# Optimization experiments

Hardware: AMD Instinct MI355X
Metric: run time of the kernel (lower is better)

Reference implementation:

```python
import jax, jax.numpy as jnp
import numpy as np

ALPHA_MIN = float(np.exp(-1.0 / 5.0))
ALPHA_MAX = float(np.exp(-1.0 / 25.0))
B, T, F_IN, H = 32, 1000, 700, 512

# Boxcar surrogate spike: forward heaviside, backward pass-through on |x|<=0.5
@jax.custom_vjp
def spike(x):
    return (x > 0).astype(x.dtype)

def _spike_fwd(x):
    return (x > 0).astype(x.dtype), x

def _spike_bwd(x, g):
    return (jnp.where(jnp.abs(x) <= 0.5, g, jnp.zeros_like(g)),)

spike.defvjp(_spike_fwd, _spike_bwd)

def _ortho(k, n):
    a = jax.random.normal(k, (n, n))
    q, r = jnp.linalg.qr(a)
    return (q * jnp.sign(jnp.diag(r))[None, :]).astype(jnp.float32)

def setup_inputs() -> dict:
    key = jax.random.key(0)
    ks = jax.random.split(key, 14)
    return {
        "x": jax.random.normal(ks[0], (B, T, F_IN), dtype=jnp.float32),
        "W0": jax.random.normal(ks[1], (H, F_IN), dtype=jnp.float32) / np.sqrt(F_IN),
        "V0": _ortho(ks[2], H),
        "alpha0": jax.random.uniform(ks[3], (H,), minval=ALPHA_MIN, maxval=ALPHA_MAX, dtype=jnp.float32),
        "W1": jax.random.normal(ks[4], (H, H), dtype=jnp.float32) / np.sqrt(H),
        "V1": _ortho(ks[5], H),
        "alpha1": jax.random.uniform(ks[6], (H,), minval=ALPHA_MIN, maxval=ALPHA_MAX, dtype=jnp.float32),
        "Wr": jax.random.normal(ks[7], (H, H), dtype=jnp.float32) / np.sqrt(H),
        "alphar": jax.random.uniform(ks[8], (H,), minval=ALPHA_MIN, maxval=ALPHA_MAX, dtype=jnp.float32),
        "ut0_0": jax.random.uniform(ks[9], (B, H), dtype=jnp.float32),
        "st0_0": jax.random.uniform(ks[10], (B, H), dtype=jnp.float32),
        "ut0_1": jax.random.uniform(ks[11], (B, H), dtype=jnp.float32),
        "st0_1": jax.random.uniform(ks[12], (B, H), dtype=jnp.float32),
        "ut0_r": jax.random.uniform(ks[13], (B, H), dtype=jnp.float32),
    }

def _rlif(Wx, V, alpha, ut0, st0):
    # Wx: [B, T, H]; recurrent V with zeroed diagonal, st @ V as in torch source
    a = jnp.clip(alpha, ALPHA_MIN, ALPHA_MAX)
    Vz = V * (1.0 - jnp.eye(V.shape[0], dtype=V.dtype))
    def step(carry, wx_t):
        ut, st = carry
        ut = a * (ut - st) + (1.0 - a) * (wx_t + st @ Vz)
        st = spike(ut - 1.0)  # threshold = 1.0
        return (ut, st), st
    _, s = jax.lax.scan(step, (ut0, st0), jnp.swapaxes(Wx, 0, 1))  # [T, B, H]
    return jnp.swapaxes(s, 0, 1)  # [B, T, H]

def _readout(Wx, alpha, ut0):
    a = jnp.clip(alpha, ALPHA_MIN, ALPHA_MAX)
    def step(ut, wx_t):
        ut = a * ut + (1.0 - a) * wx_t
        return ut, jax.nn.softmax(ut, axis=-1)
    _, ps = jax.lax.scan(step, ut0, jnp.swapaxes(Wx, 0, 1))
    return ps.sum(axis=0)  # [B, H]

def reference(x, W0, V0, alpha0, W1, V1, alpha1, Wr, alphar, ut0_0, st0_0, ut0_1, st0_1, ut0_r):
    s0 = _rlif(jnp.einsum('btf,hf->bth', x, W0), V0, alpha0, ut0_0, st0_0)
    s1 = _rlif(jnp.einsum('bth,gh->btg', s0, W1), V1, alpha1, ut0_1, st0_1)
    out = _readout(jnp.einsum('bth,gh->btg', s1, Wr), alphar, ut0_r)
    firing_rates = jnp.concatenate([s0, s1], axis=2).mean(axis=(0, 1))  # [2H]
    return out, firing_rates
```

## Files before the change

### kernel.cpp

```cpp
#include <hip/hip_runtime.h>

#define H_   512
#define T_   1000
#define B_   32
#define FIN_ 700
#define C_   50
#define L_   20
#define PF_  4

typedef _Float16 h2v __attribute__((ext_vector_type(2)));
typedef _Float16 h4v __attribute__((ext_vector_type(4)));

static __device__ __forceinline__ float clampAlpha(float a) {
    const float AMIN = 0.8187307530779818f;
    const float AMAX = 0.9607894391523232f;
    return fminf(fmaxf(a, AMIN), AMAX);
}

__global__ __launch_bounds__(256) void vconv_kernel(
    const float* __restrict__ V, _Float16* __restrict__ Vh)
{
    const int i = (blockIdx.x * 256 + threadIdx.x) * 4;
    const float4 v = *reinterpret_cast<const float4*>(V + i);
    h4v o;
    o.x = (_Float16)v.x; o.y = (_Float16)v.y;
    o.z = (_Float16)v.z; o.w = (_Float16)v.w;
    *reinterpret_cast<h4v*>(Vh + i) = o;
}

__global__ __launch_bounds__(256) void gemm_bt_kernel(
    const float* __restrict__ A, const float* __restrict__ Bt,
    float* __restrict__ C, int M, int N, int K)
{
    __shared__ __align__(16) float As[16][68];
    __shared__ __align__(16) float Bs[16][68];
    const int tid = threadIdx.x;
    const int bm = blockIdx.x * 64;
    const int bn = blockIdx.y * 64;
    const int tx = tid & 15, ty = tid >> 4;
    const int lrow = tid >> 2;
    const int lk   = (tid & 3) << 2;
    float acc[4][4] = {};
    const float* Arow = A + (size_t)(bm + lrow) * K;
    const float* Brow = Bt + (size_t)(bn + lrow) * K;

    for (int k0 = 0; k0 < K; k0 += 16) {
        const int ka = k0 + lk;
        float4 av, bv;
        if (ka + 3 < K) {
            av = *reinterpret_cast<const float4*>(Arow + ka);
            bv = *reinterpret_cast<const float4*>(Brow + ka);
        } else {
            float a_[4], b_[4];
            #pragma unroll
            for (int i = 0; i < 4; ++i) {
                a_[i] = (ka + i < K) ? Arow[ka + i] : 0.f;
                b_[i] = (ka + i < K) ? Brow[ka + i] : 0.f;
            }
            av = make_float4(a_[0], a_[1], a_[2], a_[3]);
            bv = make_float4(b_[0], b_[1], b_[2], b_[3]);
        }
        __syncthreads();
        As[lk + 0][lrow] = av.x; As[lk + 1][lrow] = av.y;
        As[lk + 2][lrow] = av.z; As[lk + 3][lrow] = av.w;
        Bs[lk + 0][lrow] = bv.x; Bs[lk + 1][lrow] = bv.y;
        Bs[lk + 2][lrow] = bv.z; Bs[lk + 3][lrow] = bv.w;
        __syncthreads();
        #pragma unroll
        for (int kk = 0; kk < 16; ++kk) {
            const float4 a4 = *reinterpret_cast<const float4*>(&As[kk][ty << 2]);
            const float4 b4 = *reinterpret_cast<const float4*>(&Bs[kk][tx << 2]);
            const float aa[4] = {a4.x, a4.y, a4.z, a4.w};
            const float bb[4] = {b4.x, b4.y, b4.z, b4.w};
            #pragma unroll
            for (int i = 0; i < 4; ++i)
                #pragma unroll
                for (int j = 0; j < 4; ++j)
                    acc[i][j] = fmaf(aa[i], bb[j], acc[i][j]);
        }
    }
    #pragma unroll
    for (int i = 0; i < 4; ++i) {
        const float4 r = make_float4(acc[i][0], acc[i][1], acc[i][2], acc[i][3]);
        *reinterpret_cast<float4*>(&C[(size_t)(bm + ty * 4 + i) * N + bn + tx * 4]) = r;
    }
}

__global__ __launch_bounds__(256) void rlif_kernel(
    const float* __restrict__ Wx,
    const _Float16* __restrict__ Vh,
    const float* __restrict__ alpha,
    const float* __restrict__ ut0,
    const float* __restrict__ st0,
    float* __restrict__ s_out,
    float* __restrict__ fire)
{
    const int b    = blockIdx.x;
    const int tid  = threadIdx.x;
    const int j0   = tid * 2;
    const int wid  = tid >> 6;
    const int lane = tid & 63;
    __shared__ __align__(16) int act[2][4][132];
    __shared__ int cnt[2][4];
    __shared__ float st0_sh[H_];

    const float a0 = clampAlpha(alpha[j0]);
    const float a1 = clampAlpha(alpha[j0 + 1]);
    const float om0 = 1.f - a0, om1 = 1.f - a1;
    const float vd0 = (float)Vh[(size_t)j0 * H_ + j0];
    const float vd1 = (float)Vh[(size_t)(j0 + 1) * H_ + (j0 + 1)];
    float u0 = ut0[b * H_ + j0], u1 = ut0[b * H_ + j0 + 1];
    float s0 = st0[b * H_ + j0], s1 = st0[b * H_ + j0 + 1];
    float f0 = 0.f, f1 = 0.f;
    const float* wxb = Wx + (size_t)b * T_ * H_;
    float*       sob = s_out + (size_t)b * T_ * H_;

    if (tid < 8) ((int*)cnt)[tid] = 0;
    st0_sh[j0]     = st0[b * H_ + j0];
    st0_sh[j0 + 1] = st0[b * H_ + j0 + 1];
    __syncthreads();

    float pre0 = 0.f, pre1 = 0.f;
    #pragma unroll 8
    for (int h = 0; h < H_; ++h) {
        const float s = st0_sh[h];
        const h2v v = *reinterpret_cast<const h2v*>(&Vh[(size_t)h * H_ + j0]);
        pre0 = fmaf(s, (float)v.x, pre0);
        pre1 = fmaf(s, (float)v.y, pre1);
    }

    float2 wxp[PF_];
    #pragma unroll
    for (int i = 0; i < PF_; ++i)
        wxp[i] = *reinterpret_cast<const float2*>(&wxb[(size_t)i * H_ + j0]);

    int p = 0;
    for (int g = 0; g < T_ / PF_; ++g) {
        #pragma unroll
        for (int i = 0; i < PF_; ++i) {
            const int t = g * PF_ + i;
            const float2 wx = wxp[i];
            if (t + PF_ < T_)
                wxp[i] = *reinterpret_cast<const float2*>(&wxb[(size_t)(t + PF_) * H_ + j0]);

            float rec0 = 0.f, rec1 = 0.f;
            #pragma unroll
            for (int seg = 0; seg < 4; ++seg) {
                const int n = __builtin_amdgcn_readfirstlane(cnt[p][seg]);
                const int* ap = &act[p][seg][0];
                int k = 0;
                for (; k + 4 <= n; k += 4) {
                    const int4 h4 = *reinterpret_cast<const int4*>(ap + k);
                    const h2v v0 = *reinterpret_cast<const h2v*>(&Vh[(size_t)h4.x * H_ + j0]);
                    const h2v v1 = *reinterpret_cast<const h2v*>(&Vh[(size_t)h4.y * H_ + j0]);
                    const h2v v2 = *reinterpret_cast<const h2v*>(&Vh[(size_t)h4.z * H_ + j0]);
                    const h2v v3 = *reinterpret_cast<const h2v*>(&Vh[(size_t)h4.w * H_ + j0]);
                    rec0 += ((float)v0.x + (float)v1.x) + ((float)v2.x + (float)v3.x);
                    rec1 += ((float)v0.y + (float)v1.y) + ((float)v2.y + (float)v3.y);
                }
                for (; k < n; ++k) {
                    const h2v v = *reinterpret_cast<const h2v*>(&Vh[(size_t)ap[k] * H_ + j0]);
                    rec0 += (float)v.x; rec1 += (float)v.y;
                }
            }
            if (t == 0) { rec0 = pre0; rec1 = pre1; }
            rec0 -= s0 * vd0;
            rec1 -= s1 * vd1;

            u0 = a0 * (u0 - s0) + om0 * (wx.x + rec0);
            u1 = a1 * (u1 - s1) + om1 * (wx.y + rec1);
            s0 = (u0 > 1.f) ? 1.f : 0.f;
            s1 = (u1 > 1.f) ? 1.f : 0.f;
            f0 += s0; f1 += s1;
            *reinterpret_cast<float2*>(&sob[(size_t)t * H_ + j0]) = make_float2(s0, s1);

            const unsigned long long bal0 = __ballot(u0 > 1.f);
            const unsigned long long bal1 = __ballot(u1 > 1.f);
            const unsigned long long lt = (lane == 63) ? 0x7FFFFFFFFFFFFFFFULL
                                                       : ((1ULL << lane) - 1ULL);
            int k = (int)__popcll(bal0 & lt) + (int)__popcll(bal1 & lt);
            int* seg = &act[p ^ 1][wid][0];
            if (s0 != 0.f) { seg[k] = j0; ++k; }
            if (s1 != 0.f) { seg[k] = j0 + 1; }
            if (lane == 0) cnt[p ^ 1][wid] = (int)__popcll(bal0) + (int)__popcll(bal1);

            asm volatile("s_waitcnt lgkmcnt(0)" ::: "memory");
            __builtin_amdgcn_s_barrier();
            __builtin_amdgcn_sched_barrier(0);
            p ^= 1;
        }
    }
    fire[b * H_ + j0]     = f0;
    fire[b * H_ + j0 + 1] = f1;
}

__global__ __launch_bounds__(256) void ro_partial_kernel(
    const float* __restrict__ Wx,
    const float* __restrict__ alpha,
    float* __restrict__ u_end)
{
    const int b = blockIdx.x;
    const int c = blockIdx.y;
    const int j0 = threadIdx.x * 2;
    const float a0 = clampAlpha(alpha[j0]);
    const float a1 = clampAlpha(alpha[j0 + 1]);
    const float om0 = 1.f - a0, om1 = 1.f - a1;
    float u0 = 0.f, u1 = 0.f;
    const float* wxb = Wx + ((size_t)b * T_ + (size_t)c * L_) * H_;
    #pragma unroll 4
    for (int t = 0; t < L_; ++t) {
        const float2 wx = *reinterpret_cast<const float2*>(&wxb[(size_t)t * H_ + j0]);
        u0 = fmaf(a0, u0, om0 * wx.x);
        u1 = fmaf(a1, u1, om1 * wx.y);
    }
    float* ue = u_end + ((size_t)b * C_ + c) * H_;
    *reinterpret_cast<float2*>(&ue[j0]) = make_float2(u0, u1);
}

__global__ __launch_bounds__(256) void ro_carry_kernel(
    const float* __restrict__ u_end,
    const float* __restrict__ alpha,
    const float* __restrict__ ut0,
    float* __restrict__ carry)
{
    const int b = blockIdx.x;
    const int j0 = threadIdx.x * 2;
    const float a0 = clampAlpha(alpha[j0]);
    const float a1 = clampAlpha(alpha[j0 + 1]);
    const float aL0 = powf(a0, (float)L_);
    const float aL1 = powf(a1, (float)L_);
    float c0 = ut0[b * H_ + j0];
    float c1 = ut0[b * H_ + j0 + 1];
    for (int c = 0; c < C_; ++c) {
        float* cr = carry + ((size_t)b * C_ + c) * H_;
        *reinterpret_cast<float2*>(&cr[j0]) = make_float2(c0, c1);
        const float2 ue = *reinterpret_cast<const float2*>(
            &u_end[((size_t)b * C_ + c) * H_ + j0]);
        c0 = fmaf(aL0, c0, ue.x);
        c1 = fmaf(aL1, c1, ue.y);
    }
}

__global__ __launch_bounds__(256) void ro_softmax_kernel(
    const float* __restrict__ Wx,
    const float* __restrict__ alpha,
    const float* __restrict__ carry,
    float* __restrict__ opart)
{
    const int b = blockIdx.x;
    const int c = blockIdx.y;
    const int tid = threadIdx.x;
    const int j0 = tid * 2;
    __shared__ float red[8];
    const float a0 = clampAlpha(alpha[j0]);
    const float a1 = clampAlpha(alpha[j0 + 1]);
    const float om0 = 1.f - a0, om1 = 1.f - a1;
    float2 u = *reinterpret_cast<const float2*>(
        &carry[((size_t)b * C_ + c) * H_ + j0]);
    float u0 = u.x, u1 = u.y;
    float o0 = 0.f, o1 = 0.f;
    const float* wxb = Wx + ((size_t)b * T_ + (size_t)c * L_) * H_;
    const int wave = tid >> 6;
    const int lane = tid & 63;

    for (int t = 0; t < L_; ++t) {
        const float2 wx = *reinterpret_cast<const float2*>(&wxb[(size_t)t * H_ + j0]);
        u0 = fmaf(a0, u0, om0 * wx.x);
        u1 = fmaf(a1, u1, om1 * wx.y);
        float m = fmaxf(u0, u1);
        #pragma unroll
        for (int off = 32; off > 0; off >>= 1)
            m = fmaxf(m, __shfl_xor(m, off, 64));
        if (lane == 0) red[wave] = m;
        __syncthreads();
        m = fmaxf(fmaxf(red[0], red[1]), fmaxf(red[2], red[3]));
        const float e0 = expf(u0 - m), e1 = expf(u1 - m);
        float sum = e0 + e1;
        #pragma unroll
        for (int off = 32; off > 0; off >>= 1)
            sum += __shfl_xor(sum, off, 64);
        if (lane == 0) red[4 + wave] = sum;
        __syncthreads();
        sum = (red[4] + red[5]) + (red[6] + red[7]);
        const float inv = 1.f / sum;
        o0 = fmaf(e0, inv, o0);
        o1 = fmaf(e1, inv, o1);
        __syncthreads();
    }
    float* op = opart + ((size_t)c * B_ + b) * H_;
    *reinterpret_cast<float2*>(&op[j0]) = make_float2(o0, o1);
}

__global__ __launch_bounds__(256) void ro_reduce_kernel(
    const float* __restrict__ opart, float* __restrict__ out)
{
    const int idx = blockIdx.x * 256 + threadIdx.x;
    float s = 0.f;
    for (int c = 0; c < C_; ++c) s += opart[(size_t)c * B_ * H_ + idx];
    out[idx] = s;
}

__global__ __launch_bounds__(256) void fire_reduce_kernel(
    const float* __restrict__ fire, float* __restrict__ out)
{
    const int h = blockIdx.x * 256 + threadIdx.x;
    if (h >= H_) return;
    const float inv = 1.f / (float)(B_ * T_);
    float s = 0.f;
    for (int b = 0; b < B_; ++b) s += fire[b * H_ + h];
    out[h] = s * inv;
    s = 0.f;
    for (int b = 0; b < B_; ++b) s += fire[B_ * H_ + b * H_ + h];
    out[H_ + h] = s * inv;
}

extern "C" void kernel_launch(void* const* d_in, const int* in_sizes, int n_in,
                              void* d_out, int out_size, void* d_ws, size_t ws_size,
                              hipStream_t stream)
{
    const float* x      = (const float*)d_in[0];
    const float* W0     = (const float*)d_in[1];
    const float* V0     = (const float*)d_in[2];
    const float* alpha0 = (const float*)d_in[3];
    const float* W1     = (const float*)d_in[4];
    const float* V1     = (const float*)d_in[5];
    const float* alpha1 = (const float*)d_in[6];
    const float* Wr     = (const float*)d_in[7];
    const float* alphar = (const float*)d_in[8];
    const float* ut0_0  = (const float*)d_in[9];
    const float* st0_0  = (const float*)d_in[10];
    const float* ut0_1  = (const float*)d_in[11];
    const float* st0_1  = (const float*)d_in[12];
    const float* ut0_r  = (const float*)d_in[13];
    float* out = (float*)d_out;

    const size_t NBTH = (size_t)B_ * T_ * H_;
    const size_t NBCH = (size_t)B_ * C_ * H_;
    float* buf0  = (float*)d_ws;
    float* buf1  = buf0 + NBTH;
    float* fire  = buf1 + NBTH;
    float* u_end = fire + 2 * B_ * H_;
    float* carry = u_end + NBCH;
    float* opart = carry + NBCH;
    _Float16* V0h = (_Float16*)(opart + (size_t)C_ * B_ * H_);
    _Float16* V1h = V0h + (size_t)H_ * H_;

    vconv_kernel<<<(H_ * H_) / 1024, 256, 0, stream>>>(V0, V0h);
    vconv_kernel<<<(H_ * H_) / 1024, 256, 0, stream>>>(V1, V1h);

    dim3 gG(32000 / 64, 512 / 64);
    gemm_bt_kernel<<<gG, 256, 0, stream>>>(x, W0, buf0, 32000, 512, 700);
    rlif_kernel<<<32, 256, 0, stream>>>(buf0, V0h, alpha0, ut0_0, st0_0, buf1, fire);
    gemm_bt_kernel<<<gG, 256, 0, stream>>>(buf1, W1, buf0, 32000, 512, 512);
    rlif_kernel<<<32, 256, 0, stream>>>(buf0, V1h, alpha1, ut0_1, st0_1, buf1, fire + B_ * H_);
    gemm_bt_kernel<<<gG, 256, 0, stream>>>(buf1, Wr, buf0, 32000, 512, 512);
    ro_partial_kernel<<<dim3(B_, C_), 256, 0, stream>>>(buf0, alphar, u_end);
    ro_carry_kernel<<<B_, 256, 0, stream>>>(u_end, alphar, ut0_r, carry);
    ro_softmax_kernel<<<dim3(B_, C_), 256, 0, stream>>>(buf0, alphar, carry, opart);
    ro_reduce_kernel<<<(B_ * H_) / 256, 256, 0, stream>>>(opart, out);
    fire_reduce_kernel<<<2, 256, 0, stream>>>(fire, out + B_ * H_);
}
```

Baseline: 1.748 ms.

## Fuse both RLIF layers and sparse spike-driven projections into one pipelined kernel

Replaces the two per-layer RLIF kernels and the two dense GEMMs on spike tensors (W1, Wr) with one kernel. It computes layer-1 input and readout input as sparse gathers over transposed fp16 weight rows indexed by active spikes, and skews layer 1 by one step so both recurrences share a single barrier per step. This removes two 32000x512x512 GEMMs, the separate launch of the second sequential scan, and the spike-tensor writes and reads. Each step now does more gather work per thread, and W1/Wr are rounded to fp16. Workspace is reused, with the readout buffers aliasing buf0.

```diff
diff --git a/kernel.cpp b/kernel.cpp
--- a/kernel.cpp
+++ b/kernel.cpp
@@ -3,7 +3,6 @@
 #define H_   512
 #define T_   1000
 #define B_   32
-#define FIN_ 700
 #define C_   50
 #define L_   20
 #define PF_  4
@@ -26,6 +25,21 @@
     o.x = (_Float16)v.x; o.y = (_Float16)v.y;
     o.z = (_Float16)v.z; o.w = (_Float16)v.w;
     *reinterpret_cast<h4v*>(Vh + i) = o;
+}
+
+__global__ __launch_bounds__(256) void tconv_kernel(
+    const float* __restrict__ W, _Float16* __restrict__ Wt)
+{
+    __shared__ float tile[32][33];
+    const int bx = blockIdx.x * 32, by = blockIdx.y * 32;
+    const int tx = threadIdx.x & 31, ty = threadIdx.x >> 5;
+    #pragma unroll
+    for (int r = 0; r < 32; r += 8)
+        tile[ty + r][tx] = W[(size_t)(by + ty + r) * H_ + bx + tx];
+    __syncthreads();
+    #pragma unroll
+    for (int r = 0; r < 32; r += 8)
+        Wt[(size_t)(bx + ty + r) * H_ + by + tx] = (_Float16)tile[tx][ty + r];
 }
 
 __global__ __launch_bounds__(256) void gemm_bt_kernel(
@@ -86,13 +100,16 @@
     }
 }
 
-__global__ __launch_bounds__(256) void rlif_kernel(
-    const float* __restrict__ Wx,
-    const _Float16* __restrict__ Vh,
-    const float* __restrict__ alpha,
-    const float* __restrict__ ut0,
-    const float* __restrict__ st0,
-    float* __restrict__ s_out,
+__global__ __launch_bounds__(256) void fused_snn_kernel(
+    const float* __restrict__ Wx0,
+    const _Float16* __restrict__ V0h,
+    const _Float16* __restrict__ W1th,
+    const _Float16* __restrict__ V1h,
+    const _Float16* __restrict__ Wrth,
+    const float* __restrict__ alpha0, const float* __restrict__ alpha1,
+    const float* __restrict__ ut00, const float* __restrict__ st00,
+    const float* __restrict__ ut01, const float* __restrict__ st01,
+    float* __restrict__ wxr,
     float* __restrict__ fire)
 {
     const int b    = blockIdx.x;
@@ -100,34 +117,57 @@
     const int j0   = tid * 2;
     const int wid  = tid >> 6;
     const int lane = tid & 63;
-    __shared__ __align__(16) int act[2][4][132];
-    __shared__ int cnt[2][4];
-    __shared__ float st0_sh[H_];
-
-    const float a0 = clampAlpha(alpha[j0]);
-    const float a1 = clampAlpha(alpha[j0 + 1]);
-    const float om0 = 1.f - a0, om1 = 1.f - a1;
-    const float vd0 = (float)Vh[(size_t)j0 * H_ + j0];
-    const float vd1 = (float)Vh[(size_t)(j0 + 1) * H_ + (j0 + 1)];
-    float u0 = ut0[b * H_ + j0], u1 = ut0[b * H_ + j0 + 1];
-    float s0 = st0[b * H_ + j0], s1 = st0[b * H_ + j0 + 1];
-    float f0 = 0.f, f1 = 0.f;
-    const float* wxb = Wx + (size_t)b * T_ * H_;
-    float*       sob = s_out + (size_t)b * T_ * H_;
-
-    if (tid < 8) ((int*)cnt)[tid] = 0;
-    st0_sh[j0]     = st0[b * H_ + j0];
-    st0_sh[j0 + 1] = st0[b * H_ + j0 + 1];
+    __shared__ __align__(16) int act0[2][4][132];
+    __shared__ __align__(16) int act1[2][4][132];
+    __shared__ int cnt0[2][4];
+    __shared__ int cnt1[2][4];
+    __shared__ float sh[H_];
+
+    const float a0a = clampAlpha(alpha0[j0]);
+    const float a0b = clampAlpha(alpha0[j0 + 1]);
+    const float om0a = 1.f - a0a, om0b = 1.f - a0b;
+    const float a1a = clampAlpha(alpha1[j0]);
+    const float a1b = clampAlpha(alpha1[j0 + 1]);
+    const float om1a = 1.f - a1a, om1b = 1.f - a1b;
+    const float vd0a = (float)V0h[(size_t)j0 * H_ + j0];
+    const float vd0b = (float)V0h[(size_t)(j0 + 1) * H_ + j0 + 1];
+    const float vd1a = (float)V1h[(size_t)j0 * H_ + j0];
+    const float vd1b = (float)V1h[(size_t)(j0 + 1) * H_ + j0 + 1];
+
+    float u0a = ut00[b * H_ + j0], u0b = ut00[b * H_ + j0 + 1];
+    float s0a = st00[b * H_ + j0], s0b = st00[b * H_ + j0 + 1];
+    float u1a = ut01[b * H_ + j0], u1b = ut01[b * H_ + j0 + 1];
+    float s1a = st01[b * H_ + j0], s1b = st01[b * H_ + j0 + 1];
+    float f0a = 0.f, f0b = 0.f, f1a = 0.f, f1b = 0.f;
+
+    const float* wxb  = Wx0 + (size_t)b * T_ * H_;
+    float*       wxrb = wxr + (size_t)b * T_ * H_;
+
+    if (tid < 8)               ((int*)cnt0)[tid] = 0;
+    if (tid >= 8 && tid < 16)  ((int*)cnt1)[tid - 8] = 0;
+
+    sh[j0] = s0a; sh[j0 + 1] = s0b;
     __syncthreads();
-
-    float pre0 = 0.f, pre1 = 0.f;
+    float pre0a = 0.f, pre0b = 0.f;
     #pragma unroll 8
     for (int h = 0; h < H_; ++h) {
-        const float s = st0_sh[h];
-        const h2v v = *reinterpret_cast<const h2v*>(&Vh[(size_t)h * H_ + j0]);
-        pre0 = fmaf(s, (float)v.x, pre0);
-        pre1 = fmaf(s, (float)v.y, pre1);
-    }
+        const float s = sh[h];
+        const h2v v = *reinterpret_cast<const h2v*>(&V0h[(size_t)h * H_ + j0]);
+        pre0a = fmaf(s, (float)v.x, pre0a);
+        pre0b = fmaf(s, (float)v.y, pre0b);
+    }
+    __syncthreads();
+    sh[j0] = s1a; sh[j0 + 1] = s1b;
+    __syncthreads();
+    float pre1a = 0.f, pre1b = 0.f;
+    #pragma unroll 8
+    for (int h = 0; h < H_; ++h) {
+        const float s = sh[h];
+        const h2v v = *reinterpret_cast<const h2v*>(&V1h[(size_t)h * H_ + j0]);
+        pre1a = fmaf(s, (float)v.x, pre1a);
+        pre1b = fmaf(s, (float)v.y, pre1b);
+    }
+    __syncthreads();
 
     float2 wxp[PF_];
     #pragma unroll
@@ -135,54 +175,113 @@
         wxp[i] = *reinterpret_cast<const float2*>(&wxb[(size_t)i * H_ + j0]);
 
     int p = 0;
-    for (int g = 0; g < T_ / PF_; ++g) {
+    for (int g = 0; g < (T_ + 2 + PF_ - 1) / PF_; ++g) {
         #pragma unroll
-        for (int i = 0; i < PF_; ++i) {
-            const int t = g * PF_ + i;
-            const float2 wx = wxp[i];
-            if (t + PF_ < T_)
-                wxp[i] = *reinterpret_cast<const float2*>(&wxb[(size_t)(t + PF_) * H_ + j0]);
-
-            float rec0 = 0.f, rec1 = 0.f;
+        for (int i4 = 0; i4 < PF_; ++i4) {
+            const int i = g * PF_ + i4;
+            if (i > T_ + 1) break;
+
+            float r0a = 0.f, r0b = 0.f, w1a = 0.f, w1b = 0.f;
             #pragma unroll
             for (int seg = 0; seg < 4; ++seg) {
-                const int n = __builtin_amdgcn_readfirstlane(cnt[p][seg]);
-                const int* ap = &act[p][seg][0];
+                const int n = __builtin_amdgcn_readfirstlane(cnt0[p][seg]);
+                const int* ap = &act0[p][seg][0];
                 int k = 0;
                 for (; k + 4 <= n; k += 4) {
                     const int4 h4 = *reinterpret_cast<const int4*>(ap + k);
-                    const h2v v0 = *reinterpret_cast<const h2v*>(&Vh[(size_t)h4.x * H_ + j0]);
-                    const h2v v1 = *reinterpret_cast<const h2v*>(&Vh[(size_t)h4.y * H_ + j0]);
-                    const h2v v2 = *reinterpret_cast<const h2v*>(&Vh[(size_t)h4.z * H_ + j0]);
-                    const h2v v3 = *reinterpret_cast<const h2v*>(&Vh[(size_t)h4.w * H_ + j0]);
-                    rec0 += ((float)v0.x + (float)v1.x) + ((float)v2.x + (float)v3.x);
-                    rec1 += ((float)v0.y + (float)v1.y) + ((float)v2.y + (float)v3.y);
+                    const h2v va = *reinterpret_cast<const h2v*>(&V0h[(size_t)h4.x * H_ + j0]);
+                    const h2v vb = *reinterpret_cast<const h2v*>(&V0h[(size_t)h4.y * H_ + j0]);
+                    const h2v vc = *reinterpret_cast<const h2v*>(&V0h[(size_t)h4.z * H_ + j0]);
+                    const h2v vdd = *reinterpret_cast<const h2v*>(&V0h[(size_t)h4.w * H_ + j0]);
+                    const h2v wa = *reinterpret_cast<const h2v*>(&W1th[(size_t)h4.x * H_ + j0]);
+                    const h2v wb = *reinterpret_cast<const h2v*>(&W1th[(size_t)h4.y * H_ + j0]);
+                    const h2v wc = *reinterpret_cast<const h2v*>(&W1th[(size_t)h4.z * H_ + j0]);
+                    const h2v wdd = *reinterpret_cast<const h2v*>(&W1th[(size_t)h4.w * H_ + j0]);
+                    r0a += ((float)va.x + (float)vb.x) + ((float)vc.x + (float)vdd.x);
+                    r0b += ((float)va.y + (float)vb.y) + ((float)vc.y + (float)vdd.y);
+                    w1a += ((float)wa.x + (float)wb.x) + ((float)wc.x + (float)wdd.x);
+                    w1b += ((float)wa.y + (float)wb.y) + ((float)wc.y + (float)wdd.y);
                 }
                 for (; k < n; ++k) {
-                    const h2v v = *reinterpret_cast<const h2v*>(&Vh[(size_t)ap[k] * H_ + j0]);
-                    rec0 += (float)v.x; rec1 += (float)v.y;
+                    const int h = ap[k];
+                    const h2v v = *reinterpret_cast<const h2v*>(&V0h[(size_t)h * H_ + j0]);
+                    const h2v w = *reinterpret_cast<const h2v*>(&W1th[(size_t)h * H_ + j0]);
+                    r0a += (float)v.x; r0b += (float)v.y;
+                    w1a += (float)w.x; w1b += (float)w.y;
                 }
             }
-            if (t == 0) { rec0 = pre0; rec1 = pre1; }
-            rec0 -= s0 * vd0;
-            rec1 -= s1 * vd1;
-
-            u0 = a0 * (u0 - s0) + om0 * (wx.x + rec0);
-            u1 = a1 * (u1 - s1) + om1 * (wx.y + rec1);
-            s0 = (u0 > 1.f) ? 1.f : 0.f;
-            s1 = (u1 > 1.f) ? 1.f : 0.f;
-            f0 += s0; f1 += s1;
-            *reinterpret_cast<float2*>(&sob[(size_t)t * H_ + j0]) = make_float2(s0, s1);
-
-            const unsigned long long bal0 = __ballot(u0 > 1.f);
-            const unsigned long long bal1 = __ballot(u1 > 1.f);
-            const unsigned long long lt = (lane == 63) ? 0x7FFFFFFFFFFFFFFFULL
-                                                       : ((1ULL << lane) - 1ULL);
-            int k = (int)__popcll(bal0 & lt) + (int)__popcll(bal1 & lt);
-            int* seg = &act[p ^ 1][wid][0];
-            if (s0 != 0.f) { seg[k] = j0; ++k; }
-            if (s1 != 0.f) { seg[k] = j0 + 1; }
-            if (lane == 0) cnt[p ^ 1][wid] = (int)__popcll(bal0) + (int)__popcll(bal1);
+            float r1a = 0.f, r1b = 0.f, wra = 0.f, wrb = 0.f;
+            #pragma unroll
+            for (int seg = 0; seg < 4; ++seg) {
+                const int n = __builtin_amdgcn_readfirstlane(cnt1[p][seg]);
+                const int* ap = &act1[p][seg][0];
+                int k = 0;
+                for (; k + 4 <= n; k += 4) {
+                    const int4 h4 = *reinterpret_cast<const int4*>(ap + k);
+                    const h2v va = *reinterpret_cast<const h2v*>(&V1h[(size_t)h4.x * H_ + j0]);
+                    const h2v vb = *reinterpret_cast<const h2v*>(&V1h[(size_t)h4.y * H_ + j0]);
+                    const h2v vc = *reinterpret_cast<const h2v*>(&V1h[(size_t)h4.z * H_ + j0]);
+                    const h2v vdd = *reinterpret_cast<const h2v*>(&V1h[(size_t)h4.w * H_ + j0]);
+                    const h2v wa = *reinterpret_cast<const h2v*>(&Wrth[(size_t)h4.x * H_ + j0]);
+                    const h2v wb = *reinterpret_cast<const h2v*>(&Wrth[(size_t)h4.y * H_ + j0]);
+                    const h2v wc = *reinterpret_cast<const h2v*>(&Wrth[(size_t)h4.z * H_ + j0]);
+                    const h2v wdd = *reinterpret_cast<const h2v*>(&Wrth[(size_t)h4.w * H_ + j0]);
+                    r1a += ((float)va.x + (float)vb.x) + ((float)vc.x + (float)vdd.x);
+                    r1b += ((float)va.y + (float)vb.y) + ((float)vc.y + (float)vdd.y);
+                    wra += ((float)wa.x + (float)wb.x) + ((float)wc.x + (float)wdd.x);
+                    wrb += ((float)wa.y + (float)wb.y) + ((float)wc.y + (float)wdd.y);
+                }
+                for (; k < n; ++k) {
+                    const int h = ap[k];
+                    const h2v v = *reinterpret_cast<const h2v*>(&V1h[(size_t)h * H_ + j0]);
+                    const h2v w = *reinterpret_cast<const h2v*>(&Wrth[(size_t)h * H_ + j0]);
+                    r1a += (float)v.x; r1b += (float)v.y;
+                    wra += (float)w.x; wrb += (float)w.y;
+                }
+            }
+
+            if (i < T_) {
+                const float2 wx = wxp[i4];
+                if (i + PF_ < T_)
+                    wxp[i4] = *reinterpret_cast<const float2*>(&wxb[(size_t)(i + PF_) * H_ + j0]);
+                if (i == 0) { r0a = pre0a; r0b = pre0b; }
+                r0a -= s0a * vd0a; r0b -= s0b * vd0b;
+                u0a = a0a * (u0a - s0a) + om0a * (wx.x + r0a);
+                u0b = a0b * (u0b - s0b) + om0b * (wx.y + r0b);
+                s0a = (u0a > 1.f) ? 1.f : 0.f;
+                s0b = (u0b > 1.f) ? 1.f : 0.f;
+                f0a += s0a; f0b += s0b;
+                const unsigned long long ba = __ballot(u0a > 1.f);
+                const unsigned long long bb = __ballot(u0b > 1.f);
+                const unsigned long long lt = (lane == 63) ? 0x7FFFFFFFFFFFFFFFULL
+                                                           : ((1ULL << lane) - 1ULL);
+                int k = (int)__popcll(ba & lt) + (int)__popcll(bb & lt);
+                int* sp = &act0[p ^ 1][wid][0];
+                if (s0a != 0.f) { sp[k] = j0; ++k; }
+                if (s0b != 0.f) { sp[k] = j0 + 1; }
+                if (lane == 0) cnt0[p ^ 1][wid] = (int)__popcll(ba) + (int)__popcll(bb);
+            }
+            if (i >= 1 && i <= T_) {
+                if (i == 1) { r1a = pre1a; r1b = pre1b; }
+                r1a -= s1a * vd1a; r1b -= s1b * vd1b;
+                u1a = a1a * (u1a - s1a) + om1a * (w1a + r1a);
+                u1b = a1b * (u1b - s1b) + om1b * (w1b + r1b);
+                s1a = (u1a > 1.f) ? 1.f : 0.f;
+                s1b = (u1b > 1.f) ? 1.f : 0.f;
+                f1a += s1a; f1b += s1b;
+                const unsigned long long ba = __ballot(u1a > 1.f);
+                const unsigned long long bb = __ballot(u1b > 1.f);
+                const unsigned long long lt = (lane == 63) ? 0x7FFFFFFFFFFFFFFFULL
+                                                           : ((1ULL << lane) - 1ULL);
+                int k = (int)__popcll(ba & lt) + (int)__popcll(bb & lt);
+                int* sp = &act1[p ^ 1][wid][0];
+                if (s1a != 0.f) { sp[k] = j0; ++k; }
+                if (s1b != 0.f) { sp[k] = j0 + 1; }
+                if (lane == 0) cnt1[p ^ 1][wid] = (int)__popcll(ba) + (int)__popcll(bb);
+            }
+            if (i >= 2)
+                *reinterpret_cast<float2*>(&wxrb[(size_t)(i - 2) * H_ + j0]) =
+                    make_float2(wra, wrb);
 
             asm volatile("s_waitcnt lgkmcnt(0)" ::: "memory");
             __builtin_amdgcn_s_barrier();
@@ -190,13 +289,14 @@
             p ^= 1;
         }
     }
-    fire[b * H_ + j0]     = f0;
-    fire[b * H_ + j0 + 1] = f1;
+    fire[b * H_ + j0]               = f0a;
+    fire[b * H_ + j0 + 1]           = f0b;
+    fire[B_ * H_ + b * H_ + j0]     = f1a;
+    fire[B_ * H_ + b * H_ + j0 + 1] = f1b;
 }
 
 __global__ __launch_bounds__(256) void ro_partial_kernel(
-    const float* __restrict__ Wx,
-    const float* __restrict__ alpha,
+    const float* __restrict__ Wx, const float* __restrict__ alpha,
     float* __restrict__ u_end)
 {
     const int b = blockIdx.x;
@@ -218,10 +318,8 @@
 }
 
 __global__ __launch_bounds__(256) void ro_carry_kernel(
-    const float* __restrict__ u_end,
-    const float* __restrict__ alpha,
-    const float* __restrict__ ut0,
-    float* __restrict__ carry)
+    const float* __restrict__ u_end, const float* __restrict__ alpha,
+    const float* __restrict__ ut0, float* __restrict__ carry)
 {
     const int b = blockIdx.x;
     const int j0 = threadIdx.x * 2;
@@ -242,10 +340,8 @@
 }
 
 __global__ __launch_bounds__(256) void ro_softmax_kernel(
-    const float* __restrict__ Wx,
-    const float* __restrict__ alpha,
-    const float* __restrict__ carry,
-    float* __restrict__ opart)
+    const float* __restrict__ Wx, const float* __restrict__ alpha,
+    const float* __restrict__ carry, float* __restrict__ opart)
 {
     const int b = blockIdx.x;
     const int c = blockIdx.y;
@@ -336,27 +432,32 @@
 
     const size_t NBTH = (size_t)B_ * T_ * H_;
     const size_t NBCH = (size_t)B_ * C_ * H_;
-    float* buf0  = (float*)d_ws;
-    float* buf1  = buf0 + NBTH;
-    float* fire  = buf1 + NBTH;
-    float* u_end = fire + 2 * B_ * H_;
+    float* buf0 = (float*)d_ws;
+    float* buf1 = buf0 + NBTH;
+    float* fire = buf1 + NBTH;
+    _Float16* V0h  = (_Float16*)(fire + 2 * B_ * H_);
+    _Float16* V1h  = V0h + (size_t)H_ * H_;
+    _Float16* W1th = V1h + (size_t)H_ * H_;
+    _Float16* Wrth = W1th + (size_t)H_ * H_;
+    float* u_end = buf0;
     float* carry = u_end + NBCH;
     float* opart = carry + NBCH;
-    _Float16* V0h = (_Float16*)(opart + (size_t)C_ * B_ * H_);
-    _Float16* V1h = V0h + (size_t)H_ * H_;
 
     vconv_kernel<<<(H_ * H_) / 1024, 256, 0, stream>>>(V0, V0h);
     vconv_kernel<<<(H_ * H_) / 1024, 256, 0, stream>>>(V1, V1h);
+    tconv_kernel<<<dim3(16, 16), 256, 0, stream>>>(W1, W1th);
+    tconv_kernel<<<dim3(16, 16), 256, 0, stream>>>(Wr, Wrth);
 
     dim3 gG(32000 / 64, 512 / 64);
     gemm_bt_kernel<<<gG, 256, 0, stream>>>(x, W0, buf0, 32000, 512, 700);
-    rlif_kernel<<<32, 256, 0, stream>>>(buf0, V0h, alpha0, ut0_0, st0_0, buf1, fire);
-    gemm_bt_kernel<<<gG, 256, 0, stream>>>(buf1, W1, buf0, 32000, 512, 512);
-    rlif_kernel<<<32, 256, 0, stream>>>(buf0, V1h, alpha1, ut0_1, st0_1, buf1, fire + B_ * H_);
-    gemm_bt_kernel<<<gG, 256, 0, stream>>>(buf1, Wr, buf0, 32000, 512, 512);
-    ro_partial_kernel<<<dim3(B_, C_), 256, 0, stream>>>(buf0, alphar, u_end);
+
+    fused_snn_kernel<<<32, 256, 0, stream>>>(
+        buf0, V0h, W1th, V1h, Wrth, alpha0, alpha1,
+        ut0_0, st0_0, ut0_1, st0_1, buf1, fire);
+
+    ro_partial_kernel<<<dim3(B_, C_), 256, 0, stream>>>(buf1, alphar, u_end);
     ro_carry_kernel<<<B_, 256, 0, stream>>>(u_end, alphar, ut0_r, carry);
-    ro_softmax_kernel<<<dim3(B_, C_), 256, 0, stream>>>(buf0, alphar, carry, opart);
+    ro_softmax_kernel<<<dim3(B_, C_), 256, 0, stream>>>(buf1, alphar, carry, opart);
     ro_reduce_kernel<<<(B_ * H_) / 256, 256, 0, stream>>>(opart, out);
     fire_reduce_kernel<<<2, 256, 0, stream>>>(fire, out + B_ * H_);
 }
```

Result: faster. 1.405 ms (-19.6%).
